# Kernel optimization log

Measured on AMD Instinct MI355X. Metric: run time of the kernel, lower is better.

The kernel has to match this reference:

```python
import jax, jax.numpy as jnp
import numpy as np
import math

D_MODEL = 1024
NUM_HEADS = 16
D_K = D_MODEL // NUM_HEADS
SEQ = 4096
BATCH = 1
NUM_BUCKETS = 32
MAX_DISTANCE = 4096


def _relative_position_bucket(relative_position):
    # T5-style unidirectional bucketing (only k < q gets nonzero bucket)
    n = jnp.maximum(-relative_position, 0)
    max_exact = NUM_BUCKETS // 2
    is_small = n < max_exact
    nf = jnp.maximum(n, 1).astype(jnp.float32)  # avoid log(0); masked by is_small
    val_if_large = max_exact + (
        jnp.log(nf / max_exact) / math.log(MAX_DISTANCE / max_exact) * (NUM_BUCKETS - max_exact)
    ).astype(jnp.int32)
    val_if_large = jnp.minimum(val_if_large, NUM_BUCKETS - 1)
    return jnp.where(is_small, n, val_if_large)


def setup_inputs() -> dict:
    key = jax.random.key(0)
    ks = jax.random.split(key, 12)
    s = 1.0 / math.sqrt(D_MODEL)
    inp = {
        "query": jax.random.normal(ks[0], (BATCH, SEQ, D_MODEL), jnp.float32),
        "key": jax.random.normal(ks[1], (BATCH, SEQ, D_MODEL), jnp.float32),
        "value": jax.random.normal(ks[2], (BATCH, SEQ, D_MODEL), jnp.float32),
        # causal mask: True where attention is forbidden (j > i)
        "mask": jnp.triu(jnp.ones((SEQ, SEQ), bool), k=1)[None, None],
        "Wq": jax.random.normal(ks[3], (D_MODEL, D_MODEL), jnp.float32) * s,
        "bq": jnp.zeros((D_MODEL,), jnp.float32),
        "Wk": jax.random.normal(ks[4], (D_MODEL, D_MODEL), jnp.float32) * s,
        "bk": jnp.zeros((D_MODEL,), jnp.float32),
        "Wv": jax.random.normal(ks[5], (D_MODEL, D_MODEL), jnp.float32) * s,
        "bv": jnp.zeros((D_MODEL,), jnp.float32),
        "Wo": jax.random.normal(ks[6], (D_MODEL, D_MODEL), jnp.float32) * s,
        "bo": jnp.zeros((D_MODEL,), jnp.float32),
        "rpe_table": jax.random.normal(ks[7], (NUM_BUCKETS, NUM_HEADS), jnp.float32),
    }
    return inp


def reference(query, key, value, mask, Wq, bq, Wk, bk, Wv, bv, Wo, bo, rpe_table):
    B, S, _ = query.shape
    scale = jnp.sqrt(jnp.asarray(D_K, jnp.float32))

    def heads(x, W, b):  # [B,S,D] -> [B,H,S,dk]
        return (x @ W + b).reshape(B, S, NUM_HEADS, D_K).transpose(0, 2, 1, 3)

    Q = heads(query, Wq, bq)
    K = heads(key, Wk, bk)
    V = heads(value, Wv, bv)

    energy = jnp.einsum("bhqd,bhkd->bhqk", Q, K) / scale

    pos = jnp.arange(S)
    rel = pos[None, :] - pos[:, None]              # [S,S] = k_pos - q_pos
    bucket = _relative_position_bucket(rel)        # [S,S] int
    bias = rpe_table[bucket]                       # [S,S,H]
    energy = energy + bias.transpose(2, 0, 1)[None]  # [1,H,S,S]

    neg = jnp.finfo(energy.dtype).min
    energy = jnp.where(mask, neg, energy)

    attn = jax.nn.softmax(energy, axis=-1)         # dropout p=0 -> identity
    x = jnp.einsum("bhqk,bhkd->bhqd", attn, V)
    x = x.transpose(0, 2, 1, 3).reshape(B, S, D_MODEL)
    return x @ Wo + bo
```

## Files before the change

kernel.cpp:

```cpp
#include <hip/hip_runtime.h>
#include <hip/hip_bf16.h>
#include <stdint.h>

using bf16   = __hip_bfloat16;
using bf16x8 = __attribute__((ext_vector_type(8))) short;
using bf16x4 = __attribute__((ext_vector_type(4))) short;
using f32x4  = __attribute__((ext_vector_type(4))) float;
using f32x4a = __attribute__((ext_vector_type(4), aligned(4))) float;

__device__ __forceinline__ void g2l16(const void* g, void* l) {
  __builtin_amdgcn_global_load_lds(
      (const __attribute__((address_space(1))) void*)g,
      (__attribute__((address_space(3))) void*)l, 16, 0, 0);
}

__device__ __forceinline__ bf16x8 load8(const float* p) {
  f32x4 a = *(const f32x4*)p;
  f32x4 b = *(const f32x4*)(p + 4);
  bf16x8 r;
  bf16* rp = (bf16*)&r;
#pragma unroll
  for (int j = 0; j < 4; ++j) rp[j]     = __float2bfloat16(a[j]);
#pragma unroll
  for (int j = 0; j < 4; ++j) rp[4 + j] = __float2bfloat16(b[j]);
  return r;
}

__global__ __launch_bounds__(256)
void cvt_bf16(const float* __restrict__ a, const float* __restrict__ b,
              const float* __restrict__ c, bf16* __restrict__ oa,
              bf16* __restrict__ ob, bf16* __restrict__ oc)
{
  const int z = blockIdx.z;
  const float* src = (z == 0) ? a : (z == 1) ? b : c;
  bf16* dst        = (z == 0) ? oa : (z == 1) ? ob : oc;
  const int i = (blockIdx.x * 256 + threadIdx.x) * 8;
  *(bf16x8*)(dst + i) = load8(src + i);
}

__global__ __launch_bounds__(256)
void transpose_w(const float* __restrict__ w0, const float* __restrict__ w1,
                 const float* __restrict__ w2, const float* __restrict__ w3,
                 bf16* __restrict__ o0, bf16* __restrict__ o1,
                 bf16* __restrict__ o2, bf16* __restrict__ o3)
{
  __shared__ float tile[32][33];
  int z = blockIdx.z;
  const float* in = (z == 0) ? w0 : (z == 1) ? w1 : (z == 2) ? w2 : w3;
  bf16* out       = (z == 0) ? o0 : (z == 1) ? o1 : (z == 2) ? o2 : o3;
  int bx = blockIdx.x * 32, by = blockIdx.y * 32;
  int tx = threadIdx.x & 31, ty = threadIdx.x >> 5;
#pragma unroll
  for (int i = 0; i < 4; ++i)
    tile[ty + i * 8][tx] = in[(size_t)(by + ty + i * 8) * 1024 + bx + tx];
  __syncthreads();
#pragma unroll
  for (int i = 0; i < 4; ++i)
    out[(size_t)(bx + ty + i * 8) * 1024 + by + tx] = __float2bfloat16(tile[tx][ty + i * 8]);
}

__global__ __launch_bounds__(256)
void build_bias(const float* __restrict__ rpe, float* __restrict__ bt)
{
  int idx = blockIdx.x * 256 + threadIdx.x;
  if (idx >= 16 * 4104) return;
  int h = idx / 4104, j = idx - h * 4104;
  int d = j - 3;
  float v = 0.f;
  if (d >= 0 && d < 4096) {
    int b;
    if (d < 16) {
      b = d;
    } else {
      const int T[15] = {23, 32, 46, 64, 91, 128, 182, 256, 363, 512,
                         725, 1024, 1449, 2048, 2897};
      int m = 0;
#pragma unroll
      for (int i = 0; i < 15; ++i) m += (d >= T[i]);
      b = 16 + m;
    }
    v = rpe[b * 16 + h] * 1.4426950408889634f;
  }
  bt[idx] = v;
}

template <typename OT>
__device__ __forceinline__ void gemm_body(const bf16* __restrict__ A,
                                          const bf16* __restrict__ Wt,
                                          const float* __restrict__ bias,
                                          OT* __restrict__ C, bool vt,
                                          bf16* As, bf16* Bs)
{
  const int tid = threadIdx.x;
  const int lane = tid & 63, wid = tid >> 6;
  const int l15 = lane & 15, lg = lane >> 4;
  const int wr = wid >> 1, wc = wid & 1;
  const int m0 = blockIdx.x * 128, n0 = blockIdx.y * 128;

  f32x4 acc[4][4];
#pragma unroll
  for (int i = 0; i < 4; ++i)
#pragma unroll
    for (int j = 0; j < 4; ++j) acc[i][j] = (f32x4){0.f, 0.f, 0.f, 0.f};

#pragma unroll 1
  for (int kt = 0; kt < 16; ++kt) {
    const int k0 = kt * 64;
    __syncthreads();
#pragma unroll
    for (int it = 0; it < 4; ++it) {
      const int o = tid * 16 + it * 4096;
      const int row = o >> 7;
      const int sl = ((o >> 4) & 7) ^ (row & 7);
      g2l16(A  + (size_t)(m0 + row) * 1024 + k0 + sl * 8, (char*)As + wid * 1024 + it * 4096);
      g2l16(Wt + (size_t)(n0 + row) * 1024 + k0 + sl * 8, (char*)Bs + wid * 1024 + it * 4096);
    }
    __syncthreads();

    bf16x8 af[2][4], bfr[2][4];
#pragma unroll
    for (int ks = 0; ks < 2; ++ks) {
      const int s8 = ks * 4 + lg;
#pragma unroll
      for (int f = 0; f < 4; ++f) {
        const int ra_ = wr * 64 + f * 16 + l15;
        af[ks][f]  = *(const bf16x8*)((const char*)As + ra_ * 128 + ((s8 ^ (ra_ & 7)) << 4));
        const int rb_ = wc * 64 + f * 16 + l15;
        bfr[ks][f] = *(const bf16x8*)((const char*)Bs + rb_ * 128 + ((s8 ^ (rb_ & 7)) << 4));
      }
    }
#pragma unroll
    for (int ks = 0; ks < 2; ++ks)
#pragma unroll
      for (int mf = 0; mf < 4; ++mf)
#pragma unroll
        for (int nf = 0; nf < 4; ++nf)
          acc[mf][nf] = __builtin_amdgcn_mfma_f32_16x16x32_bf16(
              af[ks][mf], bfr[ks][nf], acc[mf][nf], 0, 0, 0);
  }

#pragma unroll
  for (int nf = 0; nf < 4; ++nf) {
    const int col = n0 + wc * 64 + nf * 16 + l15;
    const float bv = bias[col];
#pragma unroll
    for (int mf = 0; mf < 4; ++mf) {
      const int rowb = m0 + wr * 64 + mf * 16 + lg * 4;
#pragma unroll
      for (int r = 0; r < 4; ++r) {
        const float val = acc[mf][nf][r] + bv;
        if constexpr (sizeof(OT) == 2) {
          if (vt)
            ((bf16*)C)[((size_t)(col >> 6) << 18) + ((size_t)(col & 63) << 12) + rowb + r] =
                __float2bfloat16(val);
          else
            ((bf16*)C)[(size_t)(rowb + r) * 1024 + col] = __float2bfloat16(val);
        } else {
          ((float*)C)[(size_t)(rowb + r) * 1024 + col] = val;
        }
      }
    }
  }
}

__global__ __launch_bounds__(256)
void gemm_qkv(const bf16* __restrict__ xq, const bf16* __restrict__ xk,
              const bf16* __restrict__ xv,
              const bf16* __restrict__ wqt, const bf16* __restrict__ wkt,
              const bf16* __restrict__ wvt,
              const float* __restrict__ bq, const float* __restrict__ bk,
              const float* __restrict__ bv,
              bf16* __restrict__ Q, bf16* __restrict__ K, bf16* __restrict__ VtG)
{
  __shared__ bf16 As[128 * 64], Bs[128 * 64];
  const int z = blockIdx.z;
  gemm_body<bf16>(z == 0 ? xq : z == 1 ? xk : xv,
                  z == 0 ? wqt : z == 1 ? wkt : wvt,
                  z == 0 ? bq : z == 1 ? bk : bv,
                  z == 0 ? Q : z == 1 ? K : VtG, z == 2, As, Bs);
}

__global__ __launch_bounds__(256)
void gemm_out_k(const bf16* __restrict__ A, const bf16* __restrict__ Wt,
                const float* __restrict__ bias, float* __restrict__ C)
{
  __shared__ bf16 As[128 * 64], Bs[128 * 64];
  gemm_body<float>(A, Wt, bias, C, false, As, Bs);
}

__global__ __launch_bounds__(256)
void attn_kernel(const bf16* __restrict__ Qb, const bf16* __restrict__ Kb,
                 const bf16* __restrict__ VtG, const float* __restrict__ bias_tab,
                 bf16* __restrict__ Ob)
{
  __shared__ bf16 Ks[64 * 64];
  __shared__ bf16 Vs[64 * 64];
  __shared__ bf16 Pl[4][16 * 76];

  const int tid = threadIdx.x;
  const int lane = tid & 63, wid = tid >> 6;
  const int l15 = lane & 15, lg = lane >> 4;
  const int bid = blockIdx.x;
  const int h  = bid & 15;
  const int qt = 63 - (bid >> 4);
  const int nt = qt + 1;
  const int qw = qt * 64 + wid * 16;
  const int q_abs = qw + l15;
  const float C1 = 0.125f * 1.4426950408889634f;

  const bf16* Kh = Kb + h * 64;
  const bf16* Vh = VtG + ((size_t)h << 18);
  const float* bh = bias_tab + h * 4104 + 3;
  bf16* pw = &Pl[wid][0];

  const int kr0 = tid >> 3, ks0_ = tid & 7;
  const int kr1 = (tid + 256) >> 3, ks1_ = tid & 7;

  bf16x8 qf[2];
  {
    const bf16* qp = Qb + (size_t)q_abs * 1024 + h * 64 + lg * 8;
    qf[0] = *(const bf16x8*)qp;
    qf[1] = *(const bf16x8*)(qp + 32);
  }

  f32x4 o_acc[4];
#pragma unroll
  for (int nf = 0; nf < 4; ++nf) o_acc[nf] = (f32x4){0.f, 0.f, 0.f, 0.f};
  float m_run = -1e30f, l_run = 0.f;

  bf16x8 rk0 = *(const bf16x8*)(Kh + (size_t)kr0 * 1024 + ks0_ * 8);
  bf16x8 rk1 = *(const bf16x8*)(Kh + (size_t)kr1 * 1024 + ks1_ * 8);
  bf16x8 rv0 = *(const bf16x8*)(Vh + (size_t)kr0 * 4096 + ks0_ * 8);
  bf16x8 rv1 = *(const bf16x8*)(Vh + (size_t)kr1 * 4096 + ks1_ * 8);

#pragma unroll 1
  for (int t = 0; t < nt; ++t) {
    const int k0 = t * 64;
    __syncthreads();
    {
      const int o0 = kr0 * 128 + ((ks0_ ^ (kr0 & 7)) << 4);
      const int o1 = kr1 * 128 + ((ks1_ ^ (kr1 & 7)) << 4);
      *(bf16x8*)((char*)Ks + o0) = rk0;
      *(bf16x8*)((char*)Ks + o1) = rk1;
      *(bf16x8*)((char*)Vs + o0) = rv0;
      *(bf16x8*)((char*)Vs + o1) = rv1;
    }
    __syncthreads();
    if (t + 1 < nt) {
      const int k1 = k0 + 64;
      rk0 = *(const bf16x8*)(Kh + (size_t)(k1 + kr0) * 1024 + ks0_ * 8);
      rk1 = *(const bf16x8*)(Kh + (size_t)(k1 + kr1) * 1024 + ks1_ * 8);
      rv0 = *(const bf16x8*)(Vh + (size_t)kr0 * 4096 + k1 + ks0_ * 8);
      rv1 = *(const bf16x8*)(Vh + (size_t)kr1 * 4096 + k1 + ks1_ * 8);
    }

    f32x4 st[4];
#pragma unroll
    for (int kf = 0; kf < 4; ++kf) st[kf] = (f32x4){0.f, 0.f, 0.f, 0.f};
    __builtin_amdgcn_s_setprio(1);
#pragma unroll
    for (int kf = 0; kf < 4; ++kf) {
      const int row = kf * 16 + l15;
#pragma unroll
      for (int ks = 0; ks < 2; ++ks) {
        const int s8 = ks * 4 + lg;
        bf16x8 kfr = *(const bf16x8*)((const char*)Ks + row * 128 + ((s8 ^ (row & 7)) << 4));
        st[kf] = __builtin_amdgcn_mfma_f32_16x16x32_bf16(kfr, qf[ks], st[kf], 0, 0, 0);
      }
    }
    __builtin_amdgcn_s_setprio(0);

    float mt = -1e30f;
#pragma unroll
    for (int kf = 0; kf < 4; ++kf) {
      const int dtop = q_abs - (k0 + kf * 16 + lg * 4);
      f32x4a b4 = (f32x4a){0.f, 0.f, 0.f, 0.f};
      if (dtop >= 0) b4 = *(const f32x4a*)(bh + dtop - 3);
#pragma unroll
      for (int r = 0; r < 4; ++r) {
        const float bb = (dtop - r >= 0) ? b4[3 - r] : -1e30f;
        const float sv = st[kf][r] * C1 + bb;
        st[kf][r] = sv;
        mt = fmaxf(mt, sv);
      }
    }
    mt = fmaxf(mt, __shfl_xor(mt, 16, 64));
    mt = fmaxf(mt, __shfl_xor(mt, 32, 64));

    if (__any(mt > m_run + 11.0f)) {
      const float newm = fmaxf(m_run, mt);
      const float sc = (m_run > -1e29f) ? exp2f(m_run - newm) : 0.f;
      m_run = newm;
      float scr[4];
#pragma unroll
      for (int r = 0; r < 4; ++r) scr[r] = __shfl(sc, lg * 4 + r, 64);
#pragma unroll
      for (int nf = 0; nf < 4; ++nf)
#pragma unroll
        for (int r = 0; r < 4; ++r) o_acc[nf][r] *= scr[r];
      l_run *= sc;
    }

    float rs = 0.f;
    bf16x4 pk[4];
#pragma unroll
    for (int kf = 0; kf < 4; ++kf)
#pragma unroll
      for (int r = 0; r < 4; ++r) {
        const float p = (st[kf][r] > -1e29f) ? exp2f(st[kf][r] - m_run) : 0.f;
        ((bf16*)&pk[kf])[r] = __float2bfloat16(p);
        rs += p;
      }
    rs += __shfl_xor(rs, 16, 64);
    rs += __shfl_xor(rs, 32, 64);
    l_run += rs;

#pragma unroll
    for (int kf = 0; kf < 4; ++kf)
      *(bf16x4*)&pw[l15 * 76 + kf * 16 + lg * 4] = pk[kf];

    bf16x8 pf[2];
#pragma unroll
    for (int ks2 = 0; ks2 < 2; ++ks2)
      pf[ks2] = *(const bf16x8*)&pw[l15 * 76 + ks2 * 32 + lg * 8];
    __builtin_amdgcn_s_setprio(1);
#pragma unroll
    for (int ks2 = 0; ks2 < 2; ++ks2)
#pragma unroll
      for (int nf = 0; nf < 4; ++nf) {
        const int row = nf * 16 + l15;
        const int s8 = ks2 * 4 + lg;
        bf16x8 vfr = *(const bf16x8*)((const char*)Vs + row * 128 + ((s8 ^ (row & 7)) << 4));
        o_acc[nf] = __builtin_amdgcn_mfma_f32_16x16x32_bf16(pf[ks2], vfr, o_acc[nf], 0, 0, 0);
      }
    __builtin_amdgcn_s_setprio(0);
  }

  const float linv = 1.f / l_run;
  float lr[4];
#pragma unroll
  for (int r = 0; r < 4; ++r) lr[r] = __shfl(linv, lg * 4 + r, 64);
#pragma unroll
  for (int nf = 0; nf < 4; ++nf)
#pragma unroll
    for (int r = 0; r < 4; ++r) {
      const int row = qw + lg * 4 + r;
      Ob[(size_t)row * 1024 + h * 64 + nf * 16 + l15] =
          __float2bfloat16(o_acc[nf][r] * lr[r]);
    }
}

extern "C" void kernel_launch(void* const* d_in, const int* in_sizes, int n_in,
                              void* d_out, int out_size, void* d_ws, size_t ws_size,
                              hipStream_t stream) {
  (void)in_sizes; (void)n_in; (void)out_size; (void)ws_size;
  const float* q   = (const float*)d_in[0];
  const float* k   = (const float*)d_in[1];
  const float* v   = (const float*)d_in[2];
  const float* Wq  = (const float*)d_in[4];
  const float* bq  = (const float*)d_in[5];
  const float* Wk  = (const float*)d_in[6];
  const float* bk  = (const float*)d_in[7];
  const float* Wv  = (const float*)d_in[8];
  const float* bv  = (const float*)d_in[9];
  const float* Wo  = (const float*)d_in[10];
  const float* bo  = (const float*)d_in[11];
  const float* rpe = (const float*)d_in[12];
  float* out = (float*)d_out;

  char* ws = (char*)d_ws;
  bf16* WqT   = (bf16*)(ws + (size_t)0);
  bf16* WkT   = (bf16*)(ws + ((size_t)2  << 20));
  bf16* WvT   = (bf16*)(ws + ((size_t)4  << 20));
  bf16* WoT   = (bf16*)(ws + ((size_t)6  << 20));
  bf16* xq_bf = (bf16*)(ws + ((size_t)8  << 20));
  bf16* xk_bf = (bf16*)(ws + ((size_t)16 << 20));
  bf16* xv_bf = (bf16*)(ws + ((size_t)24 << 20));
  bf16* Qb    = (bf16*)(ws + ((size_t)32 << 20));
  bf16* Kb    = (bf16*)(ws + ((size_t)40 << 20));
  bf16* VtG   = (bf16*)(ws + ((size_t)48 << 20));
  float* bias_tab = (float*)(ws + ((size_t)56 << 20));
  bf16* Ob    = xq_bf;

  transpose_w<<<dim3(32, 32, 4), 256, 0, stream>>>(Wq, Wk, Wv, Wo, WqT, WkT, WvT, WoT);
  build_bias<<<dim3(257), 256, 0, stream>>>(rpe, bias_tab);
  cvt_bf16<<<dim3(2048, 1, 3), 256, 0, stream>>>(q, k, v, xq_bf, xk_bf, xv_bf);
  gemm_qkv<<<dim3(32, 8, 3), 256, 0, stream>>>(xq_bf, xk_bf, xv_bf, WqT, WkT, WvT,
                                               bq, bk, bv, Qb, Kb, VtG);
  attn_kernel<<<dim3(1024), 256, 0, stream>>>(Qb, Kb, VtG, bias_tab, Ob);
  gemm_out_k<<<dim3(32, 8), 256, 0, stream>>>(Ob, WoT, bo, out);
}
```

Baseline: 355.5 us.

## Fuse prep kernels, double attention query tile, narrow output GEMM tile

Merges the weight transpose, bias-table build and input conversion into one launch to cut launch overhead. Attention blocks now process 128 queries, each wave handling two 16-row query fragments, so every K/V tile loaded into shared memory is reused twice. The output GEMM uses a 128x64 tile so the launch has twice as many blocks. The costs are higher register pressure in attention and coarser causal load balance, since there are 512 blocks instead of 1024.

```diff
diff --git a/kernel.cpp b/kernel.cpp
--- a/kernel.cpp
+++ b/kernel.cpp
@@ -27,81 +27,79 @@
 }
 
 __global__ __launch_bounds__(256)
-void cvt_bf16(const float* __restrict__ a, const float* __restrict__ b,
-              const float* __restrict__ c, bf16* __restrict__ oa,
-              bf16* __restrict__ ob, bf16* __restrict__ oc)
+void prep(const float* __restrict__ q, const float* __restrict__ k,
+          const float* __restrict__ v,
+          bf16* __restrict__ oq, bf16* __restrict__ ok, bf16* __restrict__ ov,
+          const float* __restrict__ Wq, const float* __restrict__ Wk,
+          const float* __restrict__ Wv, const float* __restrict__ Wo,
+          bf16* __restrict__ WqT, bf16* __restrict__ WkT,
+          bf16* __restrict__ WvT, bf16* __restrict__ WoT,
+          const float* __restrict__ rpe, float* __restrict__ bt)
 {
-  const int z = blockIdx.z;
-  const float* src = (z == 0) ? a : (z == 1) ? b : c;
-  bf16* dst        = (z == 0) ? oa : (z == 1) ? ob : oc;
-  const int i = (blockIdx.x * 256 + threadIdx.x) * 8;
-  *(bf16x8*)(dst + i) = load8(src + i);
-}
-
-__global__ __launch_bounds__(256)
-void transpose_w(const float* __restrict__ w0, const float* __restrict__ w1,
-                 const float* __restrict__ w2, const float* __restrict__ w3,
-                 bf16* __restrict__ o0, bf16* __restrict__ o1,
-                 bf16* __restrict__ o2, bf16* __restrict__ o3)
-{
-  __shared__ float tile[32][33];
-  int z = blockIdx.z;
-  const float* in = (z == 0) ? w0 : (z == 1) ? w1 : (z == 2) ? w2 : w3;
-  bf16* out       = (z == 0) ? o0 : (z == 1) ? o1 : (z == 2) ? o2 : o3;
-  int bx = blockIdx.x * 32, by = blockIdx.y * 32;
-  int tx = threadIdx.x & 31, ty = threadIdx.x >> 5;
-#pragma unroll
-  for (int i = 0; i < 4; ++i)
-    tile[ty + i * 8][tx] = in[(size_t)(by + ty + i * 8) * 1024 + bx + tx];
-  __syncthreads();
-#pragma unroll
-  for (int i = 0; i < 4; ++i)
-    out[(size_t)(bx + ty + i * 8) * 1024 + by + tx] = __float2bfloat16(tile[tx][ty + i * 8]);
-}
-
-__global__ __launch_bounds__(256)
-void build_bias(const float* __restrict__ rpe, float* __restrict__ bt)
-{
-  int idx = blockIdx.x * 256 + threadIdx.x;
-  if (idx >= 16 * 4104) return;
-  int h = idx / 4104, j = idx - h * 4104;
-  int d = j - 3;
-  float v = 0.f;
-  if (d >= 0 && d < 4096) {
-    int b;
-    if (d < 16) {
-      b = d;
-    } else {
-      const int T[15] = {23, 32, 46, 64, 91, 128, 182, 256, 363, 512,
-                         725, 1024, 1449, 2048, 2897};
-      int m = 0;
-#pragma unroll
-      for (int i = 0; i < 15; ++i) m += (d >= T[i]);
-      b = 16 + m;
-    }
-    v = rpe[b * 16 + h] * 1.4426950408889634f;
-  }
-  bt[idx] = v;
-}
-
-template <typename OT>
+  const int z = blockIdx.z, x = blockIdx.x, tid = threadIdx.x;
+  if (z < 3) {
+    const float* src = (z == 0) ? q : (z == 1) ? k : v;
+    bf16* dst        = (z == 0) ? oq : (z == 1) ? ok : ov;
+    const int i = (x * 256 + tid) * 8;
+    *(bf16x8*)(dst + i) = load8(src + i);
+  } else if (z < 7) {
+    if (x >= 1024) return;
+    __shared__ float tile[32][33];
+    const float* in = (z == 3) ? Wq : (z == 4) ? Wk : (z == 5) ? Wv : Wo;
+    bf16* out       = (z == 3) ? WqT : (z == 4) ? WkT : (z == 5) ? WvT : WoT;
+    const int bx = (x & 31) * 32, by = (x >> 5) * 32;
+    const int tx = tid & 31, ty = tid >> 5;
+#pragma unroll
+    for (int i = 0; i < 4; ++i)
+      tile[ty + i * 8][tx] = in[(size_t)(by + ty + i * 8) * 1024 + bx + tx];
+    __syncthreads();
+#pragma unroll
+    for (int i = 0; i < 4; ++i)
+      out[(size_t)(bx + ty + i * 8) * 1024 + by + tx] =
+          __float2bfloat16(tile[tx][ty + i * 8]);
+  } else {
+    const int idx = x * 256 + tid;
+    if (idx >= 16 * 4104) return;
+    const int h = idx / 4104, j = idx - h * 4104;
+    const int d = j - 3;
+    float val = 0.f;
+    if (d >= 0 && d < 4096) {
+      int b;
+      if (d < 16) {
+        b = d;
+      } else {
+        const int T[15] = {23, 32, 46, 64, 91, 128, 182, 256, 363, 512,
+                           725, 1024, 1449, 2048, 2897};
+        int m = 0;
+#pragma unroll
+        for (int i = 0; i < 15; ++i) m += (d >= T[i]);
+        b = 16 + m;
+      }
+      val = rpe[b * 16 + h] * 1.4426950408889634f;
+    }
+    bt[idx] = val;
+  }
+}
+
+template <typename OT, int BN>
 __device__ __forceinline__ void gemm_body(const bf16* __restrict__ A,
                                           const bf16* __restrict__ Wt,
                                           const float* __restrict__ bias,
                                           OT* __restrict__ C, bool vt,
                                           bf16* As, bf16* Bs)
 {
+  constexpr int NF = BN / 32;
   const int tid = threadIdx.x;
   const int lane = tid & 63, wid = tid >> 6;
   const int l15 = lane & 15, lg = lane >> 4;
   const int wr = wid >> 1, wc = wid & 1;
-  const int m0 = blockIdx.x * 128, n0 = blockIdx.y * 128;
-
-  f32x4 acc[4][4];
+  const int m0 = blockIdx.x * 128, n0 = blockIdx.y * BN;
+
+  f32x4 acc[4][NF];
 #pragma unroll
   for (int i = 0; i < 4; ++i)
 #pragma unroll
-    for (int j = 0; j < 4; ++j) acc[i][j] = (f32x4){0.f, 0.f, 0.f, 0.f};
+    for (int j = 0; j < NF; ++j) acc[i][j] = (f32x4){0.f, 0.f, 0.f, 0.f};
 
 #pragma unroll 1
   for (int kt = 0; kt < 16; ++kt) {
@@ -112,20 +110,31 @@
       const int o = tid * 16 + it * 4096;
       const int row = o >> 7;
       const int sl = ((o >> 4) & 7) ^ (row & 7);
-      g2l16(A  + (size_t)(m0 + row) * 1024 + k0 + sl * 8, (char*)As + wid * 1024 + it * 4096);
-      g2l16(Wt + (size_t)(n0 + row) * 1024 + k0 + sl * 8, (char*)Bs + wid * 1024 + it * 4096);
+      g2l16(A + (size_t)(m0 + row) * 1024 + k0 + sl * 8,
+            (char*)As + wid * 1024 + it * 4096);
+    }
+#pragma unroll
+    for (int it = 0; it < BN / 32; ++it) {
+      const int o = tid * 16 + it * 4096;
+      const int row = o >> 7;
+      const int sl = ((o >> 4) & 7) ^ (row & 7);
+      g2l16(Wt + (size_t)(n0 + row) * 1024 + k0 + sl * 8,
+            (char*)Bs + wid * 1024 + it * 4096);
     }
     __syncthreads();
 
-    bf16x8 af[2][4], bfr[2][4];
+    bf16x8 af[2][4], bfr[2][NF];
 #pragma unroll
     for (int ks = 0; ks < 2; ++ks) {
       const int s8 = ks * 4 + lg;
 #pragma unroll
       for (int f = 0; f < 4; ++f) {
         const int ra_ = wr * 64 + f * 16 + l15;
-        af[ks][f]  = *(const bf16x8*)((const char*)As + ra_ * 128 + ((s8 ^ (ra_ & 7)) << 4));
-        const int rb_ = wc * 64 + f * 16 + l15;
+        af[ks][f] = *(const bf16x8*)((const char*)As + ra_ * 128 + ((s8 ^ (ra_ & 7)) << 4));
+      }
+#pragma unroll
+      for (int f = 0; f < NF; ++f) {
+        const int rb_ = wc * (BN / 2) + f * 16 + l15;
         bfr[ks][f] = *(const bf16x8*)((const char*)Bs + rb_ * 128 + ((s8 ^ (rb_ & 7)) << 4));
       }
     }
@@ -134,14 +143,14 @@
 #pragma unroll
       for (int mf = 0; mf < 4; ++mf)
 #pragma unroll
-        for (int nf = 0; nf < 4; ++nf)
+        for (int nf = 0; nf < NF; ++nf)
           acc[mf][nf] = __builtin_amdgcn_mfma_f32_16x16x32_bf16(
               af[ks][mf], bfr[ks][nf], acc[mf][nf], 0, 0, 0);
   }
 
 #pragma unroll
-  for (int nf = 0; nf < 4; ++nf) {
-    const int col = n0 + wc * 64 + nf * 16 + l15;
+  for (int nf = 0; nf < NF; ++nf) {
+    const int col = n0 + wc * (BN / 2) + nf * 16 + l15;
     const float bv = bias[col];
 #pragma unroll
     for (int mf = 0; mf < 4; ++mf) {
@@ -174,18 +183,18 @@
 {
   __shared__ bf16 As[128 * 64], Bs[128 * 64];
   const int z = blockIdx.z;
-  gemm_body<bf16>(z == 0 ? xq : z == 1 ? xk : xv,
-                  z == 0 ? wqt : z == 1 ? wkt : wvt,
-                  z == 0 ? bq : z == 1 ? bk : bv,
-                  z == 0 ? Q : z == 1 ? K : VtG, z == 2, As, Bs);
+  gemm_body<bf16, 128>(z == 0 ? xq : z == 1 ? xk : xv,
+                       z == 0 ? wqt : z == 1 ? wkt : wvt,
+                       z == 0 ? bq : z == 1 ? bk : bv,
+                       z == 0 ? Q : z == 1 ? K : VtG, z == 2, As, Bs);
 }
 
 __global__ __launch_bounds__(256)
 void gemm_out_k(const bf16* __restrict__ A, const bf16* __restrict__ Wt,
                 const float* __restrict__ bias, float* __restrict__ C)
 {
-  __shared__ bf16 As[128 * 64], Bs[128 * 64];
-  gemm_body<float>(A, Wt, bias, C, false, As, Bs);
+  __shared__ bf16 As[128 * 64], Bs[64 * 64];
+  gemm_body<float, 64>(A, Wt, bias, C, false, As, Bs);
 }
 
 __global__ __launch_bounds__(256)
@@ -195,17 +204,18 @@
 {
   __shared__ bf16 Ks[64 * 64];
   __shared__ bf16 Vs[64 * 64];
-  __shared__ bf16 Pl[4][16 * 76];
+  __shared__ bf16 Pl[4][32 * 76];
 
   const int tid = threadIdx.x;
   const int lane = tid & 63, wid = tid >> 6;
   const int l15 = lane & 15, lg = lane >> 4;
   const int bid = blockIdx.x;
   const int h  = bid & 15;
-  const int qt = 63 - (bid >> 4);
-  const int nt = qt + 1;
-  const int qw = qt * 64 + wid * 16;
-  const int q_abs = qw + l15;
+  const int qt = 31 - (bid >> 4);
+  const int nt = 2 * qt + 2;
+  const int qw = qt * 128 + wid * 32;
+  const int q_abs0 = qw + l15;
+  const int q_abs1 = qw + 16 + l15;
   const float C1 = 0.125f * 1.4426950408889634f;
 
   const bf16* Kh = Kb + h * 64;
@@ -216,17 +226,21 @@
   const int kr0 = tid >> 3, ks0_ = tid & 7;
   const int kr1 = (tid + 256) >> 3, ks1_ = tid & 7;
 
-  bf16x8 qf[2];
-  {
-    const bf16* qp = Qb + (size_t)q_abs * 1024 + h * 64 + lg * 8;
-    qf[0] = *(const bf16x8*)qp;
-    qf[1] = *(const bf16x8*)(qp + 32);
-  }
-
-  f32x4 o_acc[4];
-#pragma unroll
-  for (int nf = 0; nf < 4; ++nf) o_acc[nf] = (f32x4){0.f, 0.f, 0.f, 0.f};
-  float m_run = -1e30f, l_run = 0.f;
+  bf16x8 qf[2][2];
+#pragma unroll
+  for (int qi = 0; qi < 2; ++qi) {
+    const bf16* qp = Qb + (size_t)(qw + qi * 16 + l15) * 1024 + h * 64 + lg * 8;
+    qf[qi][0] = *(const bf16x8*)qp;
+    qf[qi][1] = *(const bf16x8*)(qp + 32);
+  }
+
+  f32x4 o_acc[2][4];
+#pragma unroll
+  for (int qi = 0; qi < 2; ++qi)
+#pragma unroll
+    for (int nf = 0; nf < 4; ++nf) o_acc[qi][nf] = (f32x4){0.f, 0.f, 0.f, 0.f};
+  float m_run[2] = {-1e30f, -1e30f};
+  float l_run[2] = {0.f, 0.f};
 
   bf16x8 rk0 = *(const bf16x8*)(Kh + (size_t)kr0 * 1024 + ks0_ * 8);
   bf16x8 rk1 = *(const bf16x8*)(Kh + (size_t)kr1 * 1024 + ks1_ * 8);
@@ -254,9 +268,11 @@
       rv1 = *(const bf16x8*)(Vh + (size_t)kr1 * 4096 + k1 + ks1_ * 8);
     }
 
-    f32x4 st[4];
-#pragma unroll
-    for (int kf = 0; kf < 4; ++kf) st[kf] = (f32x4){0.f, 0.f, 0.f, 0.f};
+    f32x4 st[2][4];
+#pragma unroll
+    for (int qi = 0; qi < 2; ++qi)
+#pragma unroll
+      for (int kf = 0; kf < 4; ++kf) st[qi][kf] = (f32x4){0.f, 0.f, 0.f, 0.f};
     __builtin_amdgcn_s_setprio(1);
 #pragma unroll
     for (int kf = 0; kf < 4; ++kf) {
@@ -265,64 +281,80 @@
       for (int ks = 0; ks < 2; ++ks) {
         const int s8 = ks * 4 + lg;
         bf16x8 kfr = *(const bf16x8*)((const char*)Ks + row * 128 + ((s8 ^ (row & 7)) << 4));
-        st[kf] = __builtin_amdgcn_mfma_f32_16x16x32_bf16(kfr, qf[ks], st[kf], 0, 0, 0);
+        st[0][kf] = __builtin_amdgcn_mfma_f32_16x16x32_bf16(kfr, qf[0][ks], st[0][kf], 0, 0, 0);
+        st[1][kf] = __builtin_amdgcn_mfma_f32_16x16x32_bf16(kfr, qf[1][ks], st[1][kf], 0, 0, 0);
       }
     }
     __builtin_amdgcn_s_setprio(0);
 
-    float mt = -1e30f;
-#pragma unroll
-    for (int kf = 0; kf < 4; ++kf) {
-      const int dtop = q_abs - (k0 + kf * 16 + lg * 4);
-      f32x4a b4 = (f32x4a){0.f, 0.f, 0.f, 0.f};
-      if (dtop >= 0) b4 = *(const f32x4a*)(bh + dtop - 3);
-#pragma unroll
-      for (int r = 0; r < 4; ++r) {
-        const float bb = (dtop - r >= 0) ? b4[3 - r] : -1e30f;
-        const float sv = st[kf][r] * C1 + bb;
-        st[kf][r] = sv;
-        mt = fmaxf(mt, sv);
-      }
-    }
-    mt = fmaxf(mt, __shfl_xor(mt, 16, 64));
-    mt = fmaxf(mt, __shfl_xor(mt, 32, 64));
-
-    if (__any(mt > m_run + 11.0f)) {
-      const float newm = fmaxf(m_run, mt);
-      const float sc = (m_run > -1e29f) ? exp2f(m_run - newm) : 0.f;
-      m_run = newm;
-      float scr[4];
-#pragma unroll
-      for (int r = 0; r < 4; ++r) scr[r] = __shfl(sc, lg * 4 + r, 64);
-#pragma unroll
-      for (int nf = 0; nf < 4; ++nf)
-#pragma unroll
-        for (int r = 0; r < 4; ++r) o_acc[nf][r] *= scr[r];
-      l_run *= sc;
-    }
-
-    float rs = 0.f;
-    bf16x4 pk[4];
-#pragma unroll
-    for (int kf = 0; kf < 4; ++kf)
-#pragma unroll
-      for (int r = 0; r < 4; ++r) {
-        const float p = (st[kf][r] > -1e29f) ? exp2f(st[kf][r] - m_run) : 0.f;
-        ((bf16*)&pk[kf])[r] = __float2bfloat16(p);
-        rs += p;
-      }
-    rs += __shfl_xor(rs, 16, 64);
-    rs += __shfl_xor(rs, 32, 64);
-    l_run += rs;
-
-#pragma unroll
-    for (int kf = 0; kf < 4; ++kf)
-      *(bf16x4*)&pw[l15 * 76 + kf * 16 + lg * 4] = pk[kf];
-
-    bf16x8 pf[2];
-#pragma unroll
-    for (int ks2 = 0; ks2 < 2; ++ks2)
-      pf[ks2] = *(const bf16x8*)&pw[l15 * 76 + ks2 * 32 + lg * 8];
+    float mt[2] = {-1e30f, -1e30f};
+#pragma unroll
+    for (int qi = 0; qi < 2; ++qi) {
+      const int qa = qi ? q_abs1 : q_abs0;
+#pragma unroll
+      for (int kf = 0; kf < 4; ++kf) {
+        const int dtop = qa - (k0 + kf * 16 + lg * 4);
+        f32x4a b4 = (f32x4a){0.f, 0.f, 0.f, 0.f};
+        if (dtop >= 0) b4 = *(const f32x4a*)(bh + dtop - 3);
+#pragma unroll
+        for (int r = 0; r < 4; ++r) {
+          const float bb = (dtop - r >= 0) ? b4[3 - r] : -1e30f;
+          const float sv = st[qi][kf][r] * C1 + bb;
+          st[qi][kf][r] = sv;
+          mt[qi] = fmaxf(mt[qi], sv);
+        }
+      }
+    }
+    {
+      float a0 = __shfl_xor(mt[0], 16, 64), a1 = __shfl_xor(mt[1], 16, 64);
+      mt[0] = fmaxf(mt[0], a0); mt[1] = fmaxf(mt[1], a1);
+      a0 = __shfl_xor(mt[0], 32, 64); a1 = __shfl_xor(mt[1], 32, 64);
+      mt[0] = fmaxf(mt[0], a0); mt[1] = fmaxf(mt[1], a1);
+    }
+
+#pragma unroll
+    for (int qi = 0; qi < 2; ++qi) {
+      if (__any(mt[qi] > m_run[qi] + 11.0f)) {
+        const float newm = fmaxf(m_run[qi], mt[qi]);
+        const float sc = (m_run[qi] > -1e29f) ? exp2f(m_run[qi] - newm) : 0.f;
+        m_run[qi] = newm;
+        float scr[4];
+#pragma unroll
+        for (int r = 0; r < 4; ++r) scr[r] = __shfl(sc, lg * 4 + r, 64);
+#pragma unroll
+        for (int nf = 0; nf < 4; ++nf)
+#pragma unroll
+          for (int r = 0; r < 4; ++r) o_acc[qi][nf][r] *= scr[r];
+        l_run[qi] *= sc;
+      }
+    }
+
+#pragma unroll
+    for (int qi = 0; qi < 2; ++qi) {
+      float rs = 0.f;
+      bf16x4 pk[4];
+#pragma unroll
+      for (int kf = 0; kf < 4; ++kf)
+#pragma unroll
+        for (int r = 0; r < 4; ++r) {
+          const float p = (st[qi][kf][r] > -1e29f) ? exp2f(st[qi][kf][r] - m_run[qi]) : 0.f;
+          ((bf16*)&pk[kf])[r] = __float2bfloat16(p);
+          rs += p;
+        }
+      rs += __shfl_xor(rs, 16, 64);
+      rs += __shfl_xor(rs, 32, 64);
+      l_run[qi] += rs;
+#pragma unroll
+      for (int kf = 0; kf < 4; ++kf)
+        *(bf16x4*)&pw[(qi * 16 + l15) * 76 + kf * 16 + lg * 4] = pk[kf];
+    }
+
+    bf16x8 pf[2][2];
+#pragma unroll
+    for (int qi = 0; qi < 2; ++qi)
+#pragma unroll
+      for (int ks2 = 0; ks2 < 2; ++ks2)
+        pf[qi][ks2] = *(const bf16x8*)&pw[(qi * 16 + l15) * 76 + ks2 * 32 + lg * 8];
     __builtin_amdgcn_s_setprio(1);
 #pragma unroll
     for (int ks2 = 0; ks2 < 2; ++ks2)
@@ -331,23 +363,27 @@
         const int row = nf * 16 + l15;
         const int s8 = ks2 * 4 + lg;
         bf16x8 vfr = *(const bf16x8*)((const char*)Vs + row * 128 + ((s8 ^ (row & 7)) << 4));
-        o_acc[nf] = __builtin_amdgcn_mfma_f32_16x16x32_bf16(pf[ks2], vfr, o_acc[nf], 0, 0, 0);
+        o_acc[0][nf] = __builtin_amdgcn_mfma_f32_16x16x32_bf16(pf[0][ks2], vfr, o_acc[0][nf], 0, 0, 0);
+        o_acc[1][nf] = __builtin_amdgcn_mfma_f32_16x16x32_bf16(pf[1][ks2], vfr, o_acc[1][nf], 0, 0, 0);
       }
     __builtin_amdgcn_s_setprio(0);
   }
 
-  const float linv = 1.f / l_run;
-  float lr[4];
-#pragma unroll
-  for (int r = 0; r < 4; ++r) lr[r] = __shfl(linv, lg * 4 + r, 64);
-#pragma unroll
-  for (int nf = 0; nf < 4; ++nf)
-#pragma unroll
-    for (int r = 0; r < 4; ++r) {
-      const int row = qw + lg * 4 + r;
-      Ob[(size_t)row * 1024 + h * 64 + nf * 16 + l15] =
-          __float2bfloat16(o_acc[nf][r] * lr[r]);
-    }
+#pragma unroll
+  for (int qi = 0; qi < 2; ++qi) {
+    const float linv = 1.f / l_run[qi];
+    float lr[4];
+#pragma unroll
+    for (int r = 0; r < 4; ++r) lr[r] = __shfl(linv, lg * 4 + r, 64);
+#pragma unroll
+    for (int nf = 0; nf < 4; ++nf)
+#pragma unroll
+      for (int r = 0; r < 4; ++r) {
+        const int row = qw + qi * 16 + lg * 4 + r;
+        Ob[(size_t)row * 1024 + h * 64 + nf * 16 + l15] =
+            __float2bfloat16(o_acc[qi][nf][r] * lr[r]);
+      }
+  }
 }
 
 extern "C" void kernel_launch(void* const* d_in, const int* in_sizes, int n_in,
@@ -382,11 +418,11 @@
   float* bias_tab = (float*)(ws + ((size_t)56 << 20));
   bf16* Ob    = xq_bf;
 
-  transpose_w<<<dim3(32, 32, 4), 256, 0, stream>>>(Wq, Wk, Wv, Wo, WqT, WkT, WvT, WoT);
-  build_bias<<<dim3(257), 256, 0, stream>>>(rpe, bias_tab);
-  cvt_bf16<<<dim3(2048, 1, 3), 256, 0, stream>>>(q, k, v, xq_bf, xk_bf, xv_bf);
+  prep<<<dim3(2048, 1, 8), 256, 0, stream>>>(q, k, v, xq_bf, xk_bf, xv_bf,
+                                             Wq, Wk, Wv, Wo, WqT, WkT, WvT, WoT,
+                                             rpe, bias_tab);
   gemm_qkv<<<dim3(32, 8, 3), 256, 0, stream>>>(xq_bf, xk_bf, xv_bf, WqT, WkT, WvT,
                                                bq, bk, bv, Qb, Kb, VtG);
-  attn_kernel<<<dim3(1024), 256, 0, stream>>>(Qb, Kb, VtG, bias_tab, Ob);
-  gemm_out_k<<<dim3(32, 8), 256, 0, stream>>>(Ob, WoT, bo, out);
-}
+  attn_kernel<<<dim3(512), 256, 0, stream>>>(Qb, Kb, VtG, bias_tab, Ob);
+  gemm_out_k<<<dim3(32, 16), 256, 0, stream>>>(Ob, WoT, bo, out);
+}
```

After: 393.9 us. 1.11x slower.

## Merge prep kernels, double-buffer GEMM LDS loads, narrow output GEMM tile

Applied to the files above, without the earlier changes.

Three preprocessing kernels (input conversion, weight transpose, bias table) are merged into one launch with a z-dispatch, removing two launch gaps. The shared GEMM body now double-buffers its LDS tiles so the next K-slab's global-to-LDS loads are issued while MFMAs run on the current one, and it raises wave priority around the MFMA block. The output projection uses a 128x64 tile, doubling its block count to 512 to fill more CUs. In exchange, LDS use per block doubles, which may reduce occupancy, and the merged prep grid launches many blocks that exit immediately.

```diff
diff --git a/kernel.cpp b/kernel.cpp
--- a/kernel.cpp
+++ b/kernel.cpp
@@ -27,121 +27,144 @@
 }
 
 __global__ __launch_bounds__(256)
-void cvt_bf16(const float* __restrict__ a, const float* __restrict__ b,
-              const float* __restrict__ c, bf16* __restrict__ oa,
-              bf16* __restrict__ ob, bf16* __restrict__ oc)
+void prep(const float* __restrict__ q, const float* __restrict__ k,
+          const float* __restrict__ v,
+          bf16* __restrict__ oq, bf16* __restrict__ ok, bf16* __restrict__ ov,
+          const float* __restrict__ Wq, const float* __restrict__ Wk,
+          const float* __restrict__ Wv, const float* __restrict__ Wo,
+          bf16* __restrict__ WqT, bf16* __restrict__ WkT,
+          bf16* __restrict__ WvT, bf16* __restrict__ WoT,
+          const float* __restrict__ rpe, float* __restrict__ bt)
 {
-  const int z = blockIdx.z;
-  const float* src = (z == 0) ? a : (z == 1) ? b : c;
-  bf16* dst        = (z == 0) ? oa : (z == 1) ? ob : oc;
-  const int i = (blockIdx.x * 256 + threadIdx.x) * 8;
-  *(bf16x8*)(dst + i) = load8(src + i);
-}
-
-__global__ __launch_bounds__(256)
-void transpose_w(const float* __restrict__ w0, const float* __restrict__ w1,
-                 const float* __restrict__ w2, const float* __restrict__ w3,
-                 bf16* __restrict__ o0, bf16* __restrict__ o1,
-                 bf16* __restrict__ o2, bf16* __restrict__ o3)
-{
-  __shared__ float tile[32][33];
-  int z = blockIdx.z;
-  const float* in = (z == 0) ? w0 : (z == 1) ? w1 : (z == 2) ? w2 : w3;
-  bf16* out       = (z == 0) ? o0 : (z == 1) ? o1 : (z == 2) ? o2 : o3;
-  int bx = blockIdx.x * 32, by = blockIdx.y * 32;
-  int tx = threadIdx.x & 31, ty = threadIdx.x >> 5;
-#pragma unroll
-  for (int i = 0; i < 4; ++i)
-    tile[ty + i * 8][tx] = in[(size_t)(by + ty + i * 8) * 1024 + bx + tx];
-  __syncthreads();
-#pragma unroll
-  for (int i = 0; i < 4; ++i)
-    out[(size_t)(bx + ty + i * 8) * 1024 + by + tx] = __float2bfloat16(tile[tx][ty + i * 8]);
-}
-
-__global__ __launch_bounds__(256)
-void build_bias(const float* __restrict__ rpe, float* __restrict__ bt)
-{
-  int idx = blockIdx.x * 256 + threadIdx.x;
-  if (idx >= 16 * 4104) return;
-  int h = idx / 4104, j = idx - h * 4104;
-  int d = j - 3;
-  float v = 0.f;
-  if (d >= 0 && d < 4096) {
-    int b;
-    if (d < 16) {
-      b = d;
-    } else {
-      const int T[15] = {23, 32, 46, 64, 91, 128, 182, 256, 363, 512,
-                         725, 1024, 1449, 2048, 2897};
-      int m = 0;
-#pragma unroll
-      for (int i = 0; i < 15; ++i) m += (d >= T[i]);
-      b = 16 + m;
-    }
-    v = rpe[b * 16 + h] * 1.4426950408889634f;
+  const int z = blockIdx.z, x = blockIdx.x, tid = threadIdx.x;
+  if (z < 3) {
+    const float* src = (z == 0) ? q : (z == 1) ? k : v;
+    bf16* dst        = (z == 0) ? oq : (z == 1) ? ok : ov;
+    const int i = (x * 256 + tid) * 8;
+    *(bf16x8*)(dst + i) = load8(src + i);
+  } else if (z < 7) {
+    if (x >= 1024) return;
+    __shared__ float tile[32][33];
+    const float* in = (z == 3) ? Wq : (z == 4) ? Wk : (z == 5) ? Wv : Wo;
+    bf16* out       = (z == 3) ? WqT : (z == 4) ? WkT : (z == 5) ? WvT : WoT;
+    const int bx = (x & 31) * 32, by = (x >> 5) * 32;
+    const int tx = tid & 31, ty = tid >> 5;
+#pragma unroll
+    for (int i = 0; i < 4; ++i)
+      tile[ty + i * 8][tx] = in[(size_t)(by + ty + i * 8) * 1024 + bx + tx];
+    __syncthreads();
+#pragma unroll
+    for (int i = 0; i < 4; ++i)
+      out[(size_t)(bx + ty + i * 8) * 1024 + by + tx] =
+          __float2bfloat16(tile[tx][ty + i * 8]);
+  } else {
+    const int idx = x * 256 + tid;
+    if (idx >= 16 * 4104) return;
+    const int h = idx / 4104, j = idx - h * 4104;
+    const int d = j - 3;
+    float val = 0.f;
+    if (d >= 0 && d < 4096) {
+      int b;
+      if (d < 16) {
+        b = d;
+      } else {
+        const int T[15] = {23, 32, 46, 64, 91, 128, 182, 256, 363, 512,
+                           725, 1024, 1449, 2048, 2897};
+        int m = 0;
+#pragma unroll
+        for (int i = 0; i < 15; ++i) m += (d >= T[i]);
+        b = 16 + m;
+      }
+      val = rpe[b * 16 + h] * 1.4426950408889634f;
+    }
+    bt[idx] = val;
   }
-  bt[idx] = v;
-}
-
-template <typename OT>
+}
+
+template <typename OT, int BN>
 __device__ __forceinline__ void gemm_body(const bf16* __restrict__ A,
                                           const bf16* __restrict__ Wt,
                                           const float* __restrict__ bias,
                                           OT* __restrict__ C, bool vt,
                                           bf16* As, bf16* Bs)
 {
+  constexpr int NF = BN / 32;
+  constexpr int ABYTES = 128 * 128;
+  constexpr int BBYTES = BN * 128;
   const int tid = threadIdx.x;
   const int lane = tid & 63, wid = tid >> 6;
   const int l15 = lane & 15, lg = lane >> 4;
   const int wr = wid >> 1, wc = wid & 1;
-  const int m0 = blockIdx.x * 128, n0 = blockIdx.y * 128;
-
-  f32x4 acc[4][4];
+  const int m0 = blockIdx.x * 128, n0 = blockIdx.y * BN;
+
+  f32x4 acc[4][NF];
 #pragma unroll
   for (int i = 0; i < 4; ++i)
 #pragma unroll
-    for (int j = 0; j < 4; ++j) acc[i][j] = (f32x4){0.f, 0.f, 0.f, 0.f};
-
-#pragma unroll 1
-  for (int kt = 0; kt < 16; ++kt) {
+    for (int j = 0; j < NF; ++j) acc[i][j] = (f32x4){0.f, 0.f, 0.f, 0.f};
+
+  auto STAGE = [&](int buf, int kt) {
     const int k0 = kt * 64;
-    __syncthreads();
 #pragma unroll
     for (int it = 0; it < 4; ++it) {
       const int o = tid * 16 + it * 4096;
       const int row = o >> 7;
       const int sl = ((o >> 4) & 7) ^ (row & 7);
-      g2l16(A  + (size_t)(m0 + row) * 1024 + k0 + sl * 8, (char*)As + wid * 1024 + it * 4096);
-      g2l16(Wt + (size_t)(n0 + row) * 1024 + k0 + sl * 8, (char*)Bs + wid * 1024 + it * 4096);
-    }
-    __syncthreads();
-
-    bf16x8 af[2][4], bfr[2][4];
+      g2l16(A + (size_t)(m0 + row) * 1024 + k0 + sl * 8,
+            (char*)As + buf * ABYTES + wid * 1024 + it * 4096);
+    }
+#pragma unroll
+    for (int it = 0; it < BN / 32; ++it) {
+      const int o = tid * 16 + it * 4096;
+      const int row = o >> 7;
+      const int sl = ((o >> 4) & 7) ^ (row & 7);
+      g2l16(Wt + (size_t)(n0 + row) * 1024 + k0 + sl * 8,
+            (char*)Bs + buf * BBYTES + wid * 1024 + it * 4096);
+    }
+  };
+
+  STAGE(0, 0);
+  __syncthreads();
+  int cur = 0;
+
+#pragma unroll 1
+  for (int kt = 0; kt < 16; ++kt) {
+    if (kt + 1 < 16) STAGE(cur ^ 1, kt + 1);
+
+    const char* Ab = (const char*)As + cur * ABYTES;
+    const char* Bb = (const char*)Bs + cur * BBYTES;
+    bf16x8 af[2][4], bfr[2][NF];
 #pragma unroll
     for (int ks = 0; ks < 2; ++ks) {
       const int s8 = ks * 4 + lg;
 #pragma unroll
       for (int f = 0; f < 4; ++f) {
         const int ra_ = wr * 64 + f * 16 + l15;
-        af[ks][f]  = *(const bf16x8*)((const char*)As + ra_ * 128 + ((s8 ^ (ra_ & 7)) << 4));
-        const int rb_ = wc * 64 + f * 16 + l15;
-        bfr[ks][f] = *(const bf16x8*)((const char*)Bs + rb_ * 128 + ((s8 ^ (rb_ & 7)) << 4));
-      }
-    }
+        af[ks][f] = *(const bf16x8*)(Ab + ra_ * 128 + ((s8 ^ (ra_ & 7)) << 4));
+      }
+#pragma unroll
+      for (int f = 0; f < NF; ++f) {
+        const int rb_ = wc * (BN / 2) + f * 16 + l15;
+        bfr[ks][f] = *(const bf16x8*)(Bb + rb_ * 128 + ((s8 ^ (rb_ & 7)) << 4));
+      }
+    }
+    __builtin_amdgcn_s_setprio(1);
 #pragma unroll
     for (int ks = 0; ks < 2; ++ks)
 #pragma unroll
       for (int mf = 0; mf < 4; ++mf)
 #pragma unroll
-        for (int nf = 0; nf < 4; ++nf)
+        for (int nf = 0; nf < NF; ++nf)
           acc[mf][nf] = __builtin_amdgcn_mfma_f32_16x16x32_bf16(
               af[ks][mf], bfr[ks][nf], acc[mf][nf], 0, 0, 0);
+    __builtin_amdgcn_s_setprio(0);
+    __syncthreads();
+    cur ^= 1;
   }
 
 #pragma unroll
-  for (int nf = 0; nf < 4; ++nf) {
-    const int col = n0 + wc * 64 + nf * 16 + l15;
+  for (int nf = 0; nf < NF; ++nf) {
+    const int col = n0 + wc * (BN / 2) + nf * 16 + l15;
     const float bv = bias[col];
 #pragma unroll
     for (int mf = 0; mf < 4; ++mf) {
@@ -172,20 +195,20 @@
               const float* __restrict__ bv,
               bf16* __restrict__ Q, bf16* __restrict__ K, bf16* __restrict__ VtG)
 {
-  __shared__ bf16 As[128 * 64], Bs[128 * 64];
+  __shared__ bf16 As[2 * 128 * 64], Bs[2 * 128 * 64];
   const int z = blockIdx.z;
-  gemm_body<bf16>(z == 0 ? xq : z == 1 ? xk : xv,
-                  z == 0 ? wqt : z == 1 ? wkt : wvt,
-                  z == 0 ? bq : z == 1 ? bk : bv,
-                  z == 0 ? Q : z == 1 ? K : VtG, z == 2, As, Bs);
+  gemm_body<bf16, 128>(z == 0 ? xq : z == 1 ? xk : xv,
+                       z == 0 ? wqt : z == 1 ? wkt : wvt,
+                       z == 0 ? bq : z == 1 ? bk : bv,
+                       z == 0 ? Q : z == 1 ? K : VtG, z == 2, As, Bs);
 }
 
 __global__ __launch_bounds__(256)
 void gemm_out_k(const bf16* __restrict__ A, const bf16* __restrict__ Wt,
                 const float* __restrict__ bias, float* __restrict__ C)
 {
-  __shared__ bf16 As[128 * 64], Bs[128 * 64];
-  gemm_body<float>(A, Wt, bias, C, false, As, Bs);
+  __shared__ bf16 As[2 * 128 * 64], Bs[2 * 64 * 64];
+  gemm_body<float, 64>(A, Wt, bias, C, false, As, Bs);
 }
 
 __global__ __launch_bounds__(256)
@@ -382,11 +405,11 @@
   float* bias_tab = (float*)(ws + ((size_t)56 << 20));
   bf16* Ob    = xq_bf;
 
-  transpose_w<<<dim3(32, 32, 4), 256, 0, stream>>>(Wq, Wk, Wv, Wo, WqT, WkT, WvT, WoT);
-  build_bias<<<dim3(257), 256, 0, stream>>>(rpe, bias_tab);
-  cvt_bf16<<<dim3(2048, 1, 3), 256, 0, stream>>>(q, k, v, xq_bf, xk_bf, xv_bf);
+  prep<<<dim3(2048, 1, 8), 256, 0, stream>>>(q, k, v, xq_bf, xk_bf, xv_bf,
+                                             Wq, Wk, Wv, Wo, WqT, WkT, WvT, WoT,
+                                             rpe, bias_tab);
   gemm_qkv<<<dim3(32, 8, 3), 256, 0, stream>>>(xq_bf, xk_bf, xv_bf, WqT, WkT, WvT,
                                                bq, bk, bv, Qb, Kb, VtG);
   attn_kernel<<<dim3(1024), 256, 0, stream>>>(Qb, Kb, VtG, bias_tab, Ob);
-  gemm_out_k<<<dim3(32, 8), 256, 0, stream>>>(Ob, WoT, bo, out);
-}
+  gemm_out_k<<<dim3(32, 16), 256, 0, stream>>>(Ob, WoT, bo, out);
+}
```

Result: faster. 344.2 us (-3.2%).
